# Kernel tuning notes

Hardware: AMD Instinct MI355X
Metric: run time of the kernel (lower is better)

## Reference

```python
import jax, jax.numpy as jnp
import numpy as np

HIDDEN = 1024
INTER = 4096
N_EXPERTS = 8
TOP_K = 2
INIT_STD = 0.02


def setup_inputs() -> dict:
    key = jax.random.key(0)
    ks = jax.random.split(key, 6)
    x = jax.random.normal(ks[0], (2, 1024, HIDDEN), dtype=jnp.float32)
    Wg = jax.random.normal(ks[1], (N_EXPERTS, HIDDEN), dtype=jnp.float32) * INIT_STD
    # Expert MLP params, stacked over experts. W1: [E, H, I], W2: [E, I, H].
    W1 = jax.random.normal(ks[2], (N_EXPERTS, HIDDEN, INTER), dtype=jnp.float32) * INIT_STD
    b1 = jnp.zeros((N_EXPERTS, INTER), dtype=jnp.float32)
    W2 = jax.random.normal(ks[3], (N_EXPERTS, INTER, HIDDEN), dtype=jnp.float32) * INIT_STD
    b2 = jnp.zeros((N_EXPERTS, HIDDEN), dtype=jnp.float32)
    return {"x": x, "Wg": Wg, "W1": W1, "b1": b1, "W2": W2, "b2": b2}


def reference(x, Wg, W1, b1, W2, b2):
    orig_shape = x.shape
    xt = x.reshape(-1, HIDDEN)              # [T, H]
    T = xt.shape[0]

    # Gating: top-k logits -> softmax over the k selected experts.
    logits = xt @ Wg.T                      # [T, E]
    topk_logits, topk_idx = jax.lax.top_k(logits, TOP_K)   # [T, K]
    w = jax.nn.softmax(topk_logits, axis=-1)               # [T, K]

    # Scatter top-k weights into a dense [T, E] gate matrix (zeros elsewhere).
    rows = jnp.arange(T)[:, None]
    gates = jnp.zeros((T, N_EXPERTS), xt.dtype).at[rows, topk_idx].add(w)

    # Dense expert compute (mathematically identical: non-selected experts get
    # gate weight 0). Expert MLP: Linear -> GELU (exact, erf) -> Linear.
    h = jnp.einsum('th,ehi->tei', xt, W1) + b1             # [T, E, I]
    h = jax.nn.gelu(h, approximate=False)
    o = jnp.einsum('tei,eih->teh', h, W2) + b2             # [T, E, H]
    y = jnp.einsum('te,teh->th', gates, o)                 # [T, H]
    return y.reshape(orig_shape)
```

## Files before the change

kernel.cpp:

```cpp
#include <hip/hip_runtime.h>
#include <hip/hip_bf16.h>

#define HID 1024
#define INTER 4096
#define NE 8
#define NTOK 2048
#define MAXROWS 5120

typedef __attribute__((ext_vector_type(8))) short short8v;
typedef __attribute__((ext_vector_type(4))) short short4v;
typedef __attribute__((ext_vector_type(4))) float f32x4;

__device__ __forceinline__ unsigned short f2bf(float f) {
  unsigned int u = __builtin_bit_cast(unsigned int, f);
  u = (u + 0x7FFFu + ((u >> 16) & 1u)) >> 16;
  return (unsigned short)u;
}
__device__ __forceinline__ float bf2f(unsigned short s) {
  unsigned int u = ((unsigned int)s) << 16;
  return __builtin_bit_cast(float, u);
}

typedef const __attribute__((address_space(1))) unsigned int* gas_t;
typedef __attribute__((address_space(3))) unsigned int* las_t;
__device__ __forceinline__ void gld16(const unsigned short* g, unsigned short* l) {
  __builtin_amdgcn_global_load_lds((gas_t)(const void*)g, (las_t)(void*)l, 16, 0, 0);
}

__global__ __launch_bounds__(256) void convx_kernel(const float* __restrict__ in,
                                                    unsigned short* __restrict__ out) {
  size_t i = (size_t)blockIdx.x * 256 + threadIdx.x;
  f32x4 v = *(const f32x4*)&in[i * 4];
  uint2 r;
  r.x = (unsigned int)f2bf(v[0]) | ((unsigned int)f2bf(v[1]) << 16);
  r.y = (unsigned int)f2bf(v[2]) | ((unsigned int)f2bf(v[3]) << 16);
  *(uint2*)&out[i * 4] = r;
}

__global__ __launch_bounds__(256) void tconv_kernel(const float* __restrict__ in,
                                                    unsigned short* __restrict__ out,
                                                    int R, int C) {
  __shared__ float t[64][65];
  const int z = blockIdx.z;
  const int r0 = blockIdx.y * 64, c0 = blockIdx.x * 64;
  const int tr = threadIdx.x / 16;
  const int tc = (threadIdx.x % 16) * 4;
  const float* ip = in + ((size_t)z * R + r0) * (size_t)C + c0;
#pragma unroll
  for (int p = 0; p < 4; ++p) {
    f32x4 v = *(const f32x4*)&ip[(size_t)(p * 16 + tr) * C + tc];
    t[p * 16 + tr][tc + 0] = v[0];
    t[p * 16 + tr][tc + 1] = v[1];
    t[p * 16 + tr][tc + 2] = v[2];
    t[p * 16 + tr][tc + 3] = v[3];
  }
  __syncthreads();
  unsigned short* op = out + ((size_t)z * C + c0) * (size_t)R + r0;
#pragma unroll
  for (int p = 0; p < 4; ++p) {
    int c = p * 16 + tr;
    unsigned int a0 = (unsigned int)f2bf(t[tc + 0][c]) | ((unsigned int)f2bf(t[tc + 1][c]) << 16);
    unsigned int a1 = (unsigned int)f2bf(t[tc + 2][c]) | ((unsigned int)f2bf(t[tc + 3][c]) << 16);
    uint2 val; val.x = a0; val.y = a1;
    *(uint2*)&op[(size_t)c * R + tc] = val;
  }
}

__global__ __launch_bounds__(256) void gating_kernel(const float* __restrict__ x,
                                                     const float* __restrict__ wg,
                                                     int* __restrict__ tok_e,
                                                     float* __restrict__ tok_w) {
  const int t = blockIdx.x;
  float acc[NE];
#pragma unroll
  for (int e = 0; e < NE; ++e) acc[e] = 0.f;
  for (int k = threadIdx.x; k < HID; k += 256) {
    float xv = x[(size_t)t * HID + k];
#pragma unroll
    for (int e = 0; e < NE; ++e) acc[e] += xv * wg[e * HID + k];
  }
#pragma unroll
  for (int e = 0; e < NE; ++e) {
#pragma unroll
    for (int off = 32; off >= 1; off >>= 1) acc[e] += __shfl_xor(acc[e], off, 64);
  }
  __shared__ float red[4][NE];
  const int wave = threadIdx.x >> 6, lane = threadIdx.x & 63;
  if (lane == 0) {
#pragma unroll
    for (int e = 0; e < NE; ++e) red[wave][e] = acc[e];
  }
  __syncthreads();
  if (threadIdx.x == 0) {
    float l[NE];
#pragma unroll
    for (int e = 0; e < NE; ++e) l[e] = red[0][e] + red[1][e] + red[2][e] + red[3][e];
    int i0 = 0;
#pragma unroll
    for (int e = 1; e < NE; ++e) if (l[e] > l[i0]) i0 = e;
    int i1 = -1;
#pragma unroll
    for (int e = 0; e < NE; ++e) {
      if (e == i0) continue;
      if (i1 < 0 || l[e] > l[i1]) i1 = e;
    }
    float e1 = __expf(l[i1] - l[i0]);
    float w0 = 1.f / (1.f + e1);
    tok_e[t * 2 + 0] = i0;
    tok_e[t * 2 + 1] = i1;
    tok_w[t * 2 + 0] = w0;
    tok_w[t * 2 + 1] = 1.f - w0;
  }
}

__global__ __launch_bounds__(512) void routing_kernel(const int* __restrict__ tok_e,
                                                      int* __restrict__ list_tok,
                                                      int* __restrict__ tok_gslot,
                                                      int* __restrict__ offs_out) {
  __shared__ int cnts[NE];
  __shared__ int offs_s[NE + 1];
  const int e = threadIdx.x >> 6, lane = threadIdx.x & 63;
  int c = 0;
  for (int base = 0; base < NTOK; base += 64) {
    int tok = base + lane;
    int e0 = tok_e[tok * 2], e1 = tok_e[tok * 2 + 1];
    bool m = (e0 == e) || (e1 == e);
    unsigned long long mask = __ballot(m);
    c += __popcll(mask);
  }
  if (lane == 0) cnts[e] = c;
  __syncthreads();
  if (threadIdx.x == 0) {
    int o = 0;
    for (int i = 0; i < NE; ++i) { offs_s[i] = o; o += (cnts[i] + 127) & ~127; }
    offs_s[NE] = o;
    for (int i = 0; i <= NE; ++i) offs_out[i] = offs_s[i];
  }
  __syncthreads();
  const int off = offs_s[e];
  int run = 0;
  for (int base = 0; base < NTOK; base += 64) {
    int tok = base + lane;
    int e0 = tok_e[tok * 2], e1 = tok_e[tok * 2 + 1];
    bool m = (e0 == e) || (e1 == e);
    unsigned long long mask = __ballot(m);
    int pos = run + __popcll(mask & ((1ull << lane) - 1ull));
    if (m) {
      int gs = off + pos;
      list_tok[gs] = tok;
      tok_gslot[tok * 2 + ((e0 == e) ? 0 : 1)] = gs;
    }
    run += __popcll(mask);
  }
  const int cnt = cnts[e];
  const int padded = (cnt + 127) & ~127;
  for (int p = cnt + lane; p < padded; p += 64) list_tok[off + p] = 0;
}

template <int KTOT, int NTOT, bool FIRST, int NSPLIT>
__global__ __launch_bounds__(256, 3) void moe_gemm(const unsigned short* __restrict__ Abase,
                                                   const unsigned short* __restrict__ Bbase,
                                                   const float* __restrict__ bias,
                                                   const int* __restrict__ list_tok,
                                                   const int* __restrict__ offs,
                                                   void* __restrict__ outp) {
  constexpr int KS = KTOT / NSPLIT;
  constexpr int NT = KS / 32;
  constexpr int nM = MAXROWS / 128;
  constexpr int nN = NTOT / 128;
  __shared__ __align__(16) unsigned short lds[3][2][4096];

  const int nwg = nN * nM * NSPLIT;
  int wg = blockIdx.x;
  wg = (wg & 7) * (nwg >> 3) + (wg >> 3);
  const int ks = (NSPLIT > 1) ? (wg / (nM * nN)) : 0;
  const int rem = wg % (nM * nN);
  const int mt = rem % nM;
  const int nt = rem / nM;
  const int grow0 = mt * 128;
  if (grow0 >= offs[NE]) return;
  int e = 0;
#pragma unroll
  for (int i = 1; i < NE; ++i) if (grow0 >= offs[i]) e = i;
  const int n0 = nt * 128;
  const int k0 = ks * KS;

  const int tid = threadIdx.x;
  const int wave = tid >> 6, lane = tid & 63;

  const int srow = tid >> 2;
  const int skc = (((tid & 3) ^ ((srow >> 1) & 3)) * 8);
  const unsigned short* ag[2];
  const unsigned short* bg[2];
#pragma unroll
  for (int j = 0; j < 2; ++j) {
    const int row = srow + j * 64;
    size_t arow;
    if (FIRST) arow = (size_t)list_tok[grow0 + row] * KTOT;
    else       arow = (size_t)(grow0 + row) * KTOT;
    ag[j] = Abase + arow + k0 + skc;
    bg[j] = Bbase + (size_t)e * NTOT * KTOT + (size_t)(n0 + row) * KTOT + k0 + skc;
  }
  const int wbase = wave * 512;

  const int wm = wave >> 1, wn = wave & 1;
  const int fr = lane & 15;
  const int q = lane >> 4;
  int aoff[4], boff[4];
#pragma unroll
  for (int m = 0; m < 4; ++m) {
    const int row = wm * 64 + m * 16 + fr;
    aoff[m] = row * 32 + ((q ^ ((row >> 1) & 3)) * 8);
  }
#pragma unroll
  for (int n = 0; n < 4; ++n) {
    const int row = wn * 64 + n * 16 + fr;
    boff[n] = row * 32 + ((q ^ ((row >> 1) & 3)) * 8);
  }

  f32x4 acc[4][4] = {};

#define STAGE(S, SLOT)                                             \
  {                                                                \
    gld16(ag[0] + (S) * 32, &lds[SLOT][0][wbase]);                 \
    gld16(ag[1] + (S) * 32, &lds[SLOT][0][wbase + 2048]);          \
    gld16(bg[0] + (S) * 32, &lds[SLOT][1][wbase]);                 \
    gld16(bg[1] + (S) * 32, &lds[SLOT][1][wbase + 2048]);          \
  }

#define KITER(S, SL, DO_STAGE, VMSTR)                                 \
  {                                                                   \
    asm volatile("s_waitcnt vmcnt(" VMSTR ")" ::: "memory");          \
    asm volatile("s_barrier" ::: "memory");                           \
    const unsigned short* A = &lds[SL][0][0];                         \
    const unsigned short* B = &lds[SL][1][0];                         \
    short8v af[4], bf[4];                                             \
    _Pragma("unroll")                                                 \
    for (int m = 0; m < 4; ++m) af[m] = *(const short8v*)&A[aoff[m]]; \
    _Pragma("unroll")                                                 \
    for (int n = 0; n < 4; ++n) bf[n] = *(const short8v*)&B[boff[n]]; \
    if (DO_STAGE) {                                                   \
      int s2 = (SL) + 2; if (s2 >= 3) s2 -= 3;                        \
      STAGE((S) + 2, s2);                                             \
    }                                                                 \
    __builtin_amdgcn_s_setprio(1);                                    \
    _Pragma("unroll")                                                 \
    for (int n = 0; n < 4; ++n)                                       \
      _Pragma("unroll")                                               \
      for (int m = 0; m < 4; ++m)                                     \
        acc[m][n] = __builtin_amdgcn_mfma_f32_16x16x32_bf16(af[m], bf[n], acc[m][n], 0, 0, 0); \
    __builtin_amdgcn_s_setprio(0);                                    \
  }

  STAGE(0, 0);
  STAGE(1, 1);

  int sl = 0;
  for (int s = 0; s < NT - 2; ++s) {
    KITER(s, sl, true, "4");
    sl = sl + 1; if (sl >= 3) sl = 0;
  }
  KITER(NT - 2, sl, false, "4");
  sl = sl + 1; if (sl >= 3) sl = 0;
  KITER(NT - 1, sl, false, "0");

#undef KITER
#undef STAGE

  const int r4 = lane >> 4;
#pragma unroll
  for (int m = 0; m < 4; ++m) {
#pragma unroll
    for (int n = 0; n < 4; ++n) {
      const int gcol = n0 + wn * 64 + n * 16 + fr;
      float bv = 0.f;
      if (FIRST) bv = bias[e * NTOT + gcol];
#pragma unroll
      for (int r = 0; r < 4; ++r) {
        const int grow = grow0 + wm * 64 + m * 16 + r4 * 4 + r;
        float v = acc[m][n][r] + bv;
        if (FIRST) {
          v = 0.5f * v * (1.0f + erff(v * 0.70710678118654752f));
          ((unsigned short*)outp)[(size_t)grow * NTOT + gcol] = f2bf(v);
        } else {
          ((unsigned short*)outp)[((size_t)ks * MAXROWS + grow) * NTOT + gcol] = f2bf(v);
        }
      }
    }
  }
}

template <int NSPLIT>
__global__ __launch_bounds__(256) void combine_kernel(const unsigned short* __restrict__ part,
                                                      const int* __restrict__ tok_gslot,
                                                      const int* __restrict__ tok_e,
                                                      const float* __restrict__ tok_w,
                                                      const float* __restrict__ b2,
                                                      float* __restrict__ y) {
  const int t = blockIdx.x;
  const int c = threadIdx.x * 4;
  const int gs0 = tok_gslot[t * 2 + 0], gs1 = tok_gslot[t * 2 + 1];
  const int e0 = tok_e[t * 2 + 0], e1 = tok_e[t * 2 + 1];
  const float w0 = tok_w[t * 2 + 0], w1 = tok_w[t * 2 + 1];
  float s0[4] = {0.f, 0.f, 0.f, 0.f}, s1[4] = {0.f, 0.f, 0.f, 0.f};
#pragma unroll
  for (int ks = 0; ks < NSPLIT; ++ks) {
    short4v p0 = *(const short4v*)&part[((size_t)ks * MAXROWS + gs0) * HID + c];
    short4v p1 = *(const short4v*)&part[((size_t)ks * MAXROWS + gs1) * HID + c];
#pragma unroll
    for (int i = 0; i < 4; ++i) {
      s0[i] += bf2f((unsigned short)p0[i]);
      s1[i] += bf2f((unsigned short)p1[i]);
    }
  }
  f32x4 bb0 = *(const f32x4*)&b2[e0 * HID + c];
  f32x4 bb1 = *(const f32x4*)&b2[e1 * HID + c];
  f32x4 r;
#pragma unroll
  for (int i = 0; i < 4; ++i)
    r[i] = w0 * (s0[i] + bb0[i]) + w1 * (s1[i] + bb1[i]);
  *(f32x4*)&y[(size_t)t * HID + c] = r;
}

extern "C" void kernel_launch(void* const* d_in, const int* in_sizes, int n_in,
                              void* d_out, int out_size, void* d_ws, size_t ws_size,
                              hipStream_t stream) {
  const float* x  = (const float*)d_in[0];
  const float* wg = (const float*)d_in[1];
  const float* W1 = (const float*)d_in[2];
  const float* b1 = (const float*)d_in[3];
  const float* W2 = (const float*)d_in[4];
  const float* b2 = (const float*)d_in[5];
  float* y = (float*)d_out;

  unsigned char* ws = (unsigned char*)d_ws;
  size_t off = 0;
  unsigned short* w1t  = (unsigned short*)(ws + off);
  unsigned short* part = (unsigned short*)(ws + off); off += (size_t)NE * HID * INTER * 2;
  unsigned short* w2t  = (unsigned short*)(ws + off); off += (size_t)NE * INTER * HID * 2;
  unsigned short* xb   = (unsigned short*)(ws + off); off += (size_t)NTOK * HID * 2;
  unsigned short* h    = (unsigned short*)(ws + off); off += (size_t)MAXROWS * INTER * 2;
  int* tok_e           = (int*)(ws + off);            off += NTOK * 2 * 4;
  float* tok_w         = (float*)(ws + off);          off += NTOK * 2 * 4;
  int* tok_gslot       = (int*)(ws + off);            off += NTOK * 2 * 4;
  int* list_tok        = (int*)(ws + off);            off += MAXROWS * 4;
  int* offs            = (int*)(ws + off);            off += 64;
  (void)ws_size; (void)in_sizes; (void)n_in; (void)out_size;

  convx_kernel<<<(NTOK * HID / 4 + 255) / 256, 256, 0, stream>>>(x, xb);
  tconv_kernel<<<dim3(INTER / 64, HID / 64, NE), 256, 0, stream>>>(W1, w1t, HID, INTER);
  tconv_kernel<<<dim3(HID / 64, INTER / 64, NE), 256, 0, stream>>>(W2, w2t, INTER, HID);
  gating_kernel<<<NTOK, 256, 0, stream>>>(x, wg, tok_e, tok_w);
  routing_kernel<<<1, 512, 0, stream>>>(tok_e, list_tok, tok_gslot, offs);
  moe_gemm<HID, INTER, true, 1><<<(INTER / 128) * (MAXROWS / 128), 256, 0, stream>>>(
      xb, w1t, b1, list_tok, offs, (void*)h);
  moe_gemm<INTER, HID, false, 4><<<(HID / 128) * (MAXROWS / 128) * 4, 256, 0, stream>>>(
      h, w2t, b2, list_tok, offs, (void*)part);
  combine_kernel<4><<<NTOK, 256, 0, stream>>>(part, tok_gslot, tok_e, tok_w, b2, y);
}
```

Before: 250.9 us.

## Double-buffer MFMA register fragments and unroll K loop to overlap LDS reads

Restructures the GEMM main loop so the LDS fragment reads for the next K step go into a second register buffer while the MFMAs for the current step run. The loop is unrolled by six, which makes the triple-buffered LDS slot indices compile-time constants. Global staging for step s+2 is now issued before the wait/barrier rather than after the fragment loads. This adds register pressure from the doubled fragment arrays, and a static_assert now requires the tile-step count to be of the form 6k+2.

```diff
diff --git a/kernel.cpp b/kernel.cpp
--- a/kernel.cpp
+++ b/kernel.cpp
@@ -166,6 +166,7 @@
                                                    void* __restrict__ outp) {
   constexpr int KS = KTOT / NSPLIT;
   constexpr int NT = KS / 32;
+  static_assert(NT >= 8 && (NT - 2) % 6 == 0, "NT must be 6k+2");
   constexpr int nM = MAXROWS / 128;
   constexpr int nN = NTOT / 128;
   __shared__ __align__(16) unsigned short lds[3][2][4096];
@@ -219,6 +220,7 @@
   }
 
   f32x4 acc[4][4] = {};
+  short8v af[2][4], bf[2][4];
 
 #define STAGE(S, SLOT)                                             \
   {                                                                \
@@ -228,43 +230,54 @@
     gld16(bg[1] + (S) * 32, &lds[SLOT][1][wbase + 2048]);          \
   }
 
-#define KITER(S, SL, DO_STAGE, VMSTR)                                 \
-  {                                                                   \
-    asm volatile("s_waitcnt vmcnt(" VMSTR ")" ::: "memory");          \
-    asm volatile("s_barrier" ::: "memory");                           \
-    const unsigned short* A = &lds[SL][0][0];                         \
-    const unsigned short* B = &lds[SL][1][0];                         \
-    short8v af[4], bf[4];                                             \
-    _Pragma("unroll")                                                 \
-    for (int m = 0; m < 4; ++m) af[m] = *(const short8v*)&A[aoff[m]]; \
-    _Pragma("unroll")                                                 \
-    for (int n = 0; n < 4; ++n) bf[n] = *(const short8v*)&B[boff[n]]; \
-    if (DO_STAGE) {                                                   \
-      int s2 = (SL) + 2; if (s2 >= 3) s2 -= 3;                        \
-      STAGE((S) + 2, s2);                                             \
-    }                                                                 \
-    __builtin_amdgcn_s_setprio(1);                                    \
-    _Pragma("unroll")                                                 \
-    for (int n = 0; n < 4; ++n)                                       \
-      _Pragma("unroll")                                               \
-      for (int m = 0; m < 4; ++m)                                     \
-        acc[m][n] = __builtin_amdgcn_mfma_f32_16x16x32_bf16(af[m], bf[n], acc[m][n], 0, 0, 0); \
-    __builtin_amdgcn_s_setprio(0);                                    \
+#define READF(BK, SLN)                                                          \
+  {                                                                             \
+    _Pragma("unroll")                                                           \
+    for (int m = 0; m < 4; ++m) af[BK][m] = *(const short8v*)&lds[SLN][0][aoff[m]]; \
+    _Pragma("unroll")                                                           \
+    for (int n = 0; n < 4; ++n) bf[BK][n] = *(const short8v*)&lds[SLN][1][boff[n]]; \
+  }
+
+#define MFMAC(BK)                                                  \
+  {                                                                \
+    __builtin_amdgcn_s_setprio(1);                                 \
+    _Pragma("unroll")                                              \
+    for (int n = 0; n < 4; ++n)                                    \
+      _Pragma("unroll")                                            \
+      for (int m = 0; m < 4; ++m)                                  \
+        acc[m][n] = __builtin_amdgcn_mfma_f32_16x16x32_bf16(af[BK][m], bf[BK][n], acc[m][n], 0, 0, 0); \
+    __builtin_amdgcn_s_setprio(0);                                 \
+  }
+
+#define ITER(S, SL, CUR, DOSTAGE, VMSTR, DOREAD)                   \
+  {                                                                \
+    if (DOSTAGE) STAGE((S) + 2, (((SL) + 2) % 3));                 \
+    asm volatile("s_waitcnt vmcnt(" VMSTR ") lgkmcnt(0)" ::: "memory"); \
+    asm volatile("s_barrier" ::: "memory");                        \
+    if (DOREAD) READF(1 - (CUR), (((SL) + 1) % 3));                \
+    MFMAC(CUR);                                                    \
   }
 
   STAGE(0, 0);
   STAGE(1, 1);
-
-  int sl = 0;
-  for (int s = 0; s < NT - 2; ++s) {
-    KITER(s, sl, true, "4");
-    sl = sl + 1; if (sl >= 3) sl = 0;
-  }
-  KITER(NT - 2, sl, false, "4");
-  sl = sl + 1; if (sl >= 3) sl = 0;
-  KITER(NT - 1, sl, false, "0");
-
-#undef KITER
+  asm volatile("s_waitcnt vmcnt(4)" ::: "memory");
+  asm volatile("s_barrier" ::: "memory");
+  READF(0, 0);
+
+  for (int s = 0; s < NT - 2; s += 6) {
+    ITER(s + 0, 0, 0, true, "4", true);
+    ITER(s + 1, 1, 1, true, "4", true);
+    ITER(s + 2, 2, 0, true, "4", true);
+    ITER(s + 3, 0, 1, true, "4", true);
+    ITER(s + 4, 1, 0, true, "4", true);
+    ITER(s + 5, 2, 1, true, "4", true);
+  }
+  ITER(NT - 2, 0, 0, false, "0", true);
+  MFMAC(1);
+
+#undef ITER
+#undef MFMAC
+#undef READF
 #undef STAGE
 
   const int r4 = lane >> 4;
```

After: 251.4 us. Within noise of the previous version (+0.2%).

## Fuse prep kernels and overlap W2 transpose-convert with first expert GEMM

Applied to the files above, without the earlier changes.

Merges the x conversion, W1 transpose-convert and gating into a single prep kernel dispatched by block index. W2 transpose-convert blocks are appended to the first MoE GEMM grid, so that conversion overlaps GEMM1 execution. This removes several kernel launches and serialization gaps. In exchange, the GEMM launch carries extra non-GEMM blocks that compete for CUs, and those blocks reuse its LDS.

```diff
diff --git a/kernel.cpp b/kernel.cpp
--- a/kernel.cpp
+++ b/kernel.cpp
@@ -27,89 +27,103 @@
   __builtin_amdgcn_global_load_lds((gas_t)(const void*)g, (las_t)(void*)l, 16, 0, 0);
 }
 
-__global__ __launch_bounds__(256) void convx_kernel(const float* __restrict__ in,
-                                                    unsigned short* __restrict__ out) {
-  size_t i = (size_t)blockIdx.x * 256 + threadIdx.x;
-  f32x4 v = *(const f32x4*)&in[i * 4];
-  uint2 r;
-  r.x = (unsigned int)f2bf(v[0]) | ((unsigned int)f2bf(v[1]) << 16);
-  r.y = (unsigned int)f2bf(v[2]) | ((unsigned int)f2bf(v[3]) << 16);
-  *(uint2*)&out[i * 4] = r;
-}
-
-__global__ __launch_bounds__(256) void tconv_kernel(const float* __restrict__ in,
-                                                    unsigned short* __restrict__ out,
-                                                    int R, int C) {
-  __shared__ float t[64][65];
-  const int z = blockIdx.z;
-  const int r0 = blockIdx.y * 64, c0 = blockIdx.x * 64;
+__device__ __forceinline__ void tconv_tile(const float* __restrict__ in,
+                                           unsigned short* __restrict__ out,
+                                           int R, int C, int bx, int by, int z,
+                                           float* __restrict__ t) {
+  const int r0 = by * 64, c0 = bx * 64;
   const int tr = threadIdx.x / 16;
   const int tc = (threadIdx.x % 16) * 4;
   const float* ip = in + ((size_t)z * R + r0) * (size_t)C + c0;
 #pragma unroll
   for (int p = 0; p < 4; ++p) {
     f32x4 v = *(const f32x4*)&ip[(size_t)(p * 16 + tr) * C + tc];
-    t[p * 16 + tr][tc + 0] = v[0];
-    t[p * 16 + tr][tc + 1] = v[1];
-    t[p * 16 + tr][tc + 2] = v[2];
-    t[p * 16 + tr][tc + 3] = v[3];
+    t[(p * 16 + tr) * 65 + tc + 0] = v[0];
+    t[(p * 16 + tr) * 65 + tc + 1] = v[1];
+    t[(p * 16 + tr) * 65 + tc + 2] = v[2];
+    t[(p * 16 + tr) * 65 + tc + 3] = v[3];
   }
   __syncthreads();
   unsigned short* op = out + ((size_t)z * C + c0) * (size_t)R + r0;
 #pragma unroll
   for (int p = 0; p < 4; ++p) {
     int c = p * 16 + tr;
-    unsigned int a0 = (unsigned int)f2bf(t[tc + 0][c]) | ((unsigned int)f2bf(t[tc + 1][c]) << 16);
-    unsigned int a1 = (unsigned int)f2bf(t[tc + 2][c]) | ((unsigned int)f2bf(t[tc + 3][c]) << 16);
+    unsigned int a0 = (unsigned int)f2bf(t[(tc + 0) * 65 + c]) |
+                      ((unsigned int)f2bf(t[(tc + 1) * 65 + c]) << 16);
+    unsigned int a1 = (unsigned int)f2bf(t[(tc + 2) * 65 + c]) |
+                      ((unsigned int)f2bf(t[(tc + 3) * 65 + c]) << 16);
     uint2 val; val.x = a0; val.y = a1;
     *(uint2*)&op[(size_t)c * R + tc] = val;
   }
 }
 
-__global__ __launch_bounds__(256) void gating_kernel(const float* __restrict__ x,
-                                                     const float* __restrict__ wg,
-                                                     int* __restrict__ tok_e,
-                                                     float* __restrict__ tok_w) {
-  const int t = blockIdx.x;
-  float acc[NE];
-#pragma unroll
-  for (int e = 0; e < NE; ++e) acc[e] = 0.f;
-  for (int k = threadIdx.x; k < HID; k += 256) {
-    float xv = x[(size_t)t * HID + k];
-#pragma unroll
-    for (int e = 0; e < NE; ++e) acc[e] += xv * wg[e * HID + k];
-  }
-#pragma unroll
-  for (int e = 0; e < NE; ++e) {
-#pragma unroll
-    for (int off = 32; off >= 1; off >>= 1) acc[e] += __shfl_xor(acc[e], off, 64);
-  }
-  __shared__ float red[4][NE];
-  const int wave = threadIdx.x >> 6, lane = threadIdx.x & 63;
-  if (lane == 0) {
-#pragma unroll
-    for (int e = 0; e < NE; ++e) red[wave][e] = acc[e];
-  }
-  __syncthreads();
-  if (threadIdx.x == 0) {
-    float l[NE];
-#pragma unroll
-    for (int e = 0; e < NE; ++e) l[e] = red[0][e] + red[1][e] + red[2][e] + red[3][e];
-    int i0 = 0;
-#pragma unroll
-    for (int e = 1; e < NE; ++e) if (l[e] > l[i0]) i0 = e;
-    int i1 = -1;
+__global__ __launch_bounds__(256) void prep_kernel(const float* __restrict__ x,
+                                                   const float* __restrict__ W1,
+                                                   const float* __restrict__ wg,
+                                                   unsigned short* __restrict__ xb,
+                                                   unsigned short* __restrict__ w1t,
+                                                   int* __restrict__ tok_e,
+                                                   float* __restrict__ tok_w) {
+  __shared__ float sh[64 * 65];
+  int bid = blockIdx.x;
+  if (bid < 2048) {
+    size_t i = (size_t)bid * 256 + threadIdx.x;
+    f32x4 v = *(const f32x4*)&x[i * 4];
+    uint2 r;
+    r.x = (unsigned int)f2bf(v[0]) | ((unsigned int)f2bf(v[1]) << 16);
+    r.y = (unsigned int)f2bf(v[2]) | ((unsigned int)f2bf(v[3]) << 16);
+    *(uint2*)&xb[i * 4] = r;
+    return;
+  }
+  bid -= 2048;
+  if (bid < 8192) {
+    tconv_tile(W1, w1t, HID, INTER, bid % 64, (bid / 64) % 16, bid / 1024, sh);
+    return;
+  }
+  bid -= 8192;
+  {
+    const int t = bid;
+    float acc[NE];
+#pragma unroll
+    for (int e = 0; e < NE; ++e) acc[e] = 0.f;
+    for (int k = threadIdx.x; k < HID; k += 256) {
+      float xv = x[(size_t)t * HID + k];
+#pragma unroll
+      for (int e = 0; e < NE; ++e) acc[e] += xv * wg[e * HID + k];
+    }
 #pragma unroll
     for (int e = 0; e < NE; ++e) {
-      if (e == i0) continue;
-      if (i1 < 0 || l[e] > l[i1]) i1 = e;
-    }
-    float e1 = __expf(l[i1] - l[i0]);
-    float w0 = 1.f / (1.f + e1);
-    tok_e[t * 2 + 0] = i0;
-    tok_e[t * 2 + 1] = i1;
-    tok_w[t * 2 + 0] = w0;
-    tok_w[t * 2 + 1] = 1.f - w0;
+#pragma unroll
+      for (int off = 32; off >= 1; off >>= 1) acc[e] += __shfl_xor(acc[e], off, 64);
+    }
+    float* red = sh;
+    const int wave = threadIdx.x >> 6, lane = threadIdx.x & 63;
+    if (lane == 0) {
+#pragma unroll
+      for (int e = 0; e < NE; ++e) red[wave * NE + e] = acc[e];
+    }
+    __syncthreads();
+    if (threadIdx.x == 0) {
+      float l[NE];
+#pragma unroll
+      for (int e = 0; e < NE; ++e)
+        l[e] = red[0 * NE + e] + red[1 * NE + e] + red[2 * NE + e] + red[3 * NE + e];
+      int i0 = 0;
+#pragma unroll
+      for (int e = 1; e < NE; ++e) if (l[e] > l[i0]) i0 = e;
+      int i1 = -1;
+#pragma unroll
+      for (int e = 0; e < NE; ++e) {
+        if (e == i0) continue;
+        if (i1 < 0 || l[e] > l[i1]) i1 = e;
+      }
+      float e1 = __expf(l[i1] - l[i0]);
+      float w0 = 1.f / (1.f + e1);
+      tok_e[t * 2 + 0] = i0;
+      tok_e[t * 2 + 1] = i1;
+      tok_w[t * 2 + 0] = w0;
+      tok_w[t * 2 + 1] = 1.f - w0;
+    }
   }
 }
 
@@ -157,22 +171,31 @@
   for (int p = cnt + lane; p < padded; p += 64) list_tok[off + p] = 0;
 }
 
-template <int KTOT, int NTOT, bool FIRST, int NSPLIT>
+template <int KTOT, int NTOT, bool FIRST, int NSPLIT, int TCONVN>
 __global__ __launch_bounds__(256, 3) void moe_gemm(const unsigned short* __restrict__ Abase,
                                                    const unsigned short* __restrict__ Bbase,
                                                    const float* __restrict__ bias,
                                                    const int* __restrict__ list_tok,
                                                    const int* __restrict__ offs,
-                                                   void* __restrict__ outp) {
+                                                   void* __restrict__ outp,
+                                                   const float* __restrict__ W2f,
+                                                   unsigned short* __restrict__ w2t) {
   constexpr int KS = KTOT / NSPLIT;
   constexpr int NT = KS / 32;
   constexpr int nM = MAXROWS / 128;
   constexpr int nN = NTOT / 128;
+  constexpr int NWG_GEMM = nN * nM * NSPLIT;
   __shared__ __align__(16) unsigned short lds[3][2][4096];
 
-  const int nwg = nN * nM * NSPLIT;
+  if (TCONVN != 0 && blockIdx.x >= NWG_GEMM) {
+    int t = blockIdx.x - NWG_GEMM;
+    tconv_tile(W2f, w2t, INTER, HID, t % 16, (t / 16) % 64, t / 1024,
+               (float*)&lds[0][0][0]);
+    return;
+  }
+
   int wg = blockIdx.x;
-  wg = (wg & 7) * (nwg >> 3) + (wg >> 3);
+  wg = (wg & 7) * (NWG_GEMM >> 3) + (wg >> 3);
   const int ks = (NSPLIT > 1) ? (wg / (nM * nN)) : 0;
   const int rem = wg % (nM * nN);
   const int mt = rem % nM;
@@ -347,14 +370,13 @@
   int* offs            = (int*)(ws + off);            off += 64;
   (void)ws_size; (void)in_sizes; (void)n_in; (void)out_size;
 
-  convx_kernel<<<(NTOK * HID / 4 + 255) / 256, 256, 0, stream>>>(x, xb);
-  tconv_kernel<<<dim3(INTER / 64, HID / 64, NE), 256, 0, stream>>>(W1, w1t, HID, INTER);
-  tconv_kernel<<<dim3(HID / 64, INTER / 64, NE), 256, 0, stream>>>(W2, w2t, INTER, HID);
-  gating_kernel<<<NTOK, 256, 0, stream>>>(x, wg, tok_e, tok_w);
+  prep_kernel<<<2048 + 8192 + 2048, 256, 0, stream>>>(x, W1, wg, xb, w1t, tok_e, tok_w);
   routing_kernel<<<1, 512, 0, stream>>>(tok_e, list_tok, tok_gslot, offs);
-  moe_gemm<HID, INTER, true, 1><<<(INTER / 128) * (MAXROWS / 128), 256, 0, stream>>>(
-      xb, w1t, b1, list_tok, offs, (void*)h);
-  moe_gemm<INTER, HID, false, 4><<<(HID / 128) * (MAXROWS / 128) * 4, 256, 0, stream>>>(
-      h, w2t, b2, list_tok, offs, (void*)part);
+  moe_gemm<HID, INTER, true, 1, 8192>
+      <<<(INTER / 128) * (MAXROWS / 128) + 8192, 256, 0, stream>>>(
+          xb, w1t, b1, list_tok, offs, (void*)h, W2, w2t);
+  moe_gemm<INTER, HID, false, 4, 0>
+      <<<(HID / 128) * (MAXROWS / 128) * 4, 256, 0, stream>>>(
+          h, w2t, b2, list_tok, offs, (void*)part, nullptr, nullptr);
   combine_kernel<4><<<NTOK, 256, 0, stream>>>(part, tok_gslot, tok_e, tok_w, b2, y);
 }
```

Measured after the change: 215.2 us. 14.2% less time.
